# Kernel tuning notes

Hardware: AMD Instinct MI355X
Metric: run time of the kernel (lower is better)

Reference implementation:

```python
import jax, jax.numpy as jnp
import numpy as np

N, E, B = 100000, 200000, 4096
D, FEAT, L = 300, 512, 5
NUM_ATOM, NUM_CHI = 119, 3
NUM_BOND, NUM_DIR = 5, 3
EPS = 1e-5


def setup_inputs() -> dict:
    key = jax.random.key(0)
    ks = jax.random.split(key, 24)
    x = jax.random.randint(ks[0], (N, 2), 0, 3, dtype=jnp.int32)
    edge_index = jax.random.randint(ks[1], (2, E), 0, N, dtype=jnp.int32)
    edge_attr = jax.random.randint(ks[2], (E, 2), 0, 3, dtype=jnp.int32)
    batch = jnp.sort(jax.random.randint(ks[3], (N,), 0, B, dtype=jnp.int32))
    s = 0.02
    p = {
        'x_emb1': jax.random.normal(ks[4], (NUM_ATOM, D)) * s,
        'x_emb2': jax.random.normal(ks[5], (NUM_CHI, D)) * s,
        'edge_emb1': jax.random.normal(ks[6], (L, NUM_BOND, D)) * s,
        'edge_emb2': jax.random.normal(ks[7], (L, NUM_DIR, D)) * s,
        'W1': jax.random.normal(ks[8], (L, D, 2 * D)) * s,
        'b1': jnp.zeros((L, 2 * D)),
        'W2': jax.random.normal(ks[9], (L, 2 * D, D)) * s,
        'b2': jnp.zeros((L, D)),
        'gamma': jnp.ones((L, D)),
        'beta': jnp.zeros((L, D)),
        'W_feat': jax.random.normal(ks[10], (D, FEAT)) * s,
        'b_feat': jnp.zeros((FEAT,)),
        'Wp1': jax.random.normal(ks[11], (FEAT, FEAT // 2)) * s,
        'bp1': jnp.zeros((FEAT // 2,)),
        'Wp2': jax.random.normal(ks[12], (FEAT // 2, FEAT // 2)) * s,
        'bp2': jnp.zeros((FEAT // 2,)),
        'Wp3': jax.random.normal(ks[13], (FEAT // 2, 2)) * s,
        'bp3': jnp.zeros((2,)),
    }
    return dict(x=x, edge_index=edge_index, edge_attr=edge_attr, batch=batch, **p)


def reference(x, edge_index, edge_attr, batch, x_emb1, x_emb2, edge_emb1, edge_emb2,
              W1, b1, W2, b2, gamma, beta, W_feat, b_feat, Wp1, bp1, Wp2, bp2, Wp3, bp3):
    n = x.shape[0]
    ar = jnp.arange(n, dtype=edge_index.dtype)
    src = jnp.concatenate([edge_index[0], ar])  # [E+N] message sources
    dst = jnp.concatenate([edge_index[1], ar])  # [E+N] aggregation targets
    # self-loop edge attr: bond type 4, direction 0
    sl = jnp.stack([jnp.full((n,), 4, edge_attr.dtype), jnp.zeros((n,), edge_attr.dtype)], axis=1)
    ea = jnp.concatenate([edge_attr, sl], axis=0)  # [E+N, 2]

    h = x_emb1[x[:, 0]] + x_emb2[x[:, 1]]  # [N, D]
    for l in range(L):
        ee = edge_emb1[l][ea[:, 0]] + edge_emb2[l][ea[:, 1]]  # [E+N, D]
        msg = h[src] + ee
        aggr = jax.ops.segment_sum(msg, dst, num_segments=n)  # GIN add-aggregate
        h = jax.nn.relu(aggr @ W1[l] + b1[l]) @ W2[l] + b2[l]
        mu = h.mean(axis=0)
        var = ((h - mu) ** 2).mean(axis=0)  # biased var (torch BN training mode)
        h = (h - mu) * jax.lax.rsqrt(var + EPS) * gamma[l] + beta[l]
        if l < L - 1:
            h = jax.nn.relu(h)

    ones = jnp.ones((n,), h.dtype)
    counts = jax.ops.segment_sum(ones, batch, num_segments=B)
    pooled = jax.ops.segment_sum(h, batch, num_segments=B) / jnp.maximum(counts, 1.0)[:, None]
    hf = pooled @ W_feat + b_feat  # [B, FEAT]
    p = jax.nn.softplus(hf @ Wp1 + bp1)
    p = jax.nn.softplus(p @ Wp2 + bp2)
    pred = p @ Wp3 + bp3  # [B, 2]
    return hf, pred
```

## Files before the change

kernel.cpp:

```cpp
#include <hip/hip_runtime.h>
#include <cstdint>
#include <cstddef>

typedef unsigned short u16;
typedef __bf16 bf16x8 __attribute__((ext_vector_type(8)));
typedef float  f32x4  __attribute__((ext_vector_type(4)));

#define NN 100000
#define EE 200000
#define BG 4096
#define DV 300
#define DP 320
#define D2 600
#define D2P 640
#define FEAT 512
#define FH 256
#define NL 5
#define CHUNK 50048
#define QN (NN/4)

__device__ __forceinline__ float b2f(u16 u) {
    union { float f; unsigned int i; } x; x.i = ((unsigned int)u) << 16; return x.f;
}
__device__ __forceinline__ u16 f2b(float f) {
    union { float f; unsigned int i; } x; x.f = f;
    unsigned int r = (x.i + 0x7FFFu + ((x.i >> 16) & 1u)) >> 16;
    return (u16)r;
}
__device__ __forceinline__ float ldp(const void* p, size_t i, int m) {
    return m ? ((const float*)p)[i] : b2f(((const u16*)p)[i]);
}

__global__ void detect_kernel(const void* w1raw, int* mode) {
    if (threadIdx.x != 0 || blockIdx.x != 0) return;
    const u16* p = (const u16*)w1raw;
    int cnt = 0;
    for (int i = 0; i < 128; ++i) {
        u16 v = p[2 * i];
        int e = (v >> 7) & 0xFF;
        if (e >= 100 && e <= 135) ++cnt;
    }
    *mode = (cnt >= 100) ? 0 : 1;
}

__global__ void zero_int_kernel(int* __restrict__ p, long n) {
    long i = (long)blockIdx.x * blockDim.x + threadIdx.x;
    long stride = (long)gridDim.x * blockDim.x;
    for (; i < n; i += stride) p[i] = 0;
}

__global__ void zero_stats_kernel(float* __restrict__ a, float* __restrict__ b) {
    int t = threadIdx.x; a[t] = 0.f; b[t] = 0.f;
}

__global__ void pack_kernel(const void* __restrict__ W1, const void* __restrict__ W2,
                            const void* __restrict__ Wf, const void* __restrict__ Wp1,
                            const void* __restrict__ Wp2,
                            const void* __restrict__ b1, const void* __restrict__ b2,
                            const void* __restrict__ bfe, const void* __restrict__ bp1,
                            const void* __restrict__ bp2,
                            const void* __restrict__ eemb1, const void* __restrict__ eemb2,
                            u16* __restrict__ W1pT, u16* __restrict__ W2pT,
                            u16* __restrict__ WfT, u16* __restrict__ Wp1T, u16* __restrict__ Wp2T,
                            float* __restrict__ b1p, float* __restrict__ b2p,
                            float* __restrict__ bfp, float* __restrict__ bp1p, float* __restrict__ bp2p,
                            const int* __restrict__ modep)
{
    const int m = *modep;
    const int s1 = NL*D2P*DP, s2 = NL*DP*D2P, s3 = FEAT*DP, s4 = FH*FEAT, s5 = FH*FH;
    const int s6 = NL*D2P, s7 = NL*DP, s8 = FEAT, s9 = FH, s10 = FH;
    int idx = blockIdx.x * 256 + threadIdx.x;
    if (idx < s1) {
        int l = idx / (D2P*DP), r = idx % (D2P*DP), n = r / DP, k = r % DP;
        u16 v = 0;
        if (n < D2) {
            if (k < DV) v = f2b(ldp(W1, ((size_t)l*DV + k)*D2 + n, m));
            else if (k < DV + 8) {
                int b = k - DV;
                float acc = 0.f;
                for (int d = 0; d < DV; ++d) {
                    float e = (b < 5) ? ldp(eemb1, ((size_t)l*5 + b)*DV + d, m)
                                      : ldp(eemb2, ((size_t)l*3 + (b-5))*DV + d, m);
                    acc += e * ldp(W1, ((size_t)l*DV + d)*D2 + n, m);
                }
                v = f2b(acc);
            }
        }
        W1pT[idx] = v; return;
    } idx -= s1;
    if (idx < s2) {
        int l = idx / (DP*D2P), r = idx % (DP*D2P), n = r / D2P, k = r % D2P;
        W2pT[idx] = (n < DV && k < D2) ? f2b(ldp(W2, ((size_t)l*D2 + k)*DV + n, m)) : (u16)0; return;
    } idx -= s2;
    if (idx < s3) { int n = idx / DP, k = idx % DP;
        WfT[idx] = (k < DV) ? f2b(ldp(Wf, (size_t)k*FEAT + n, m)) : (u16)0; return; } idx -= s3;
    if (idx < s4) { int n = idx / FEAT, k = idx % FEAT;
        Wp1T[idx] = f2b(ldp(Wp1, (size_t)k*FH + n, m)); return; } idx -= s4;
    if (idx < s5) { int n = idx / FH, k = idx % FH;
        Wp2T[idx] = f2b(ldp(Wp2, (size_t)k*FH + n, m)); return; } idx -= s5;
    if (idx < s6) { int l = idx / D2P, n = idx % D2P;
        b1p[idx] = (n < D2) ? ldp(b1, l*D2 + n, m) : 0.f; return; } idx -= s6;
    if (idx < s7) { int l = idx / DP, n = idx % DP;
        b2p[idx] = (n < DV) ? ldp(b2, l*DV + n, m) : 0.f; return; } idx -= s7;
    if (idx < s8) { bfp[idx] = ldp(bfe, idx, m); return; } idx -= s8;
    if (idx < s9) { bp1p[idx] = ldp(bp1, idx, m); return; } idx -= s9;
    if (idx < s10) { bp2p[idx] = ldp(bp2, idx, m); return; }
}

__global__ void count_kernel(const int* __restrict__ ei, const int* __restrict__ ea,
                             int* __restrict__ indeg, int* __restrict__ cnt)
{
    int e = blockIdx.x * 256 + threadIdx.x;
    if (e >= EE) return;
    int dst = ei[EE + e];
    atomicAdd(&indeg[dst], 1);
    atomicAdd(&cnt[dst*8 + ea[e*2]], 1);
    atomicAdd(&cnt[dst*8 + 5 + ea[e*2+1]], 1);
}

__global__ void scan1_kernel(const int* __restrict__ in, int* __restrict__ out,
                             int* __restrict__ partials, int n)
{
    __shared__ int sm[256];
    int t = threadIdx.x, gi = blockIdx.x * 256 + t;
    int v = (gi < n) ? in[gi] : 0;
    sm[t] = v; __syncthreads();
    int acc = v;
    for (int off = 1; off < 256; off <<= 1) {
        int other = (t >= off) ? sm[t - off] : 0;
        __syncthreads();
        acc += other; sm[t] = acc;
        __syncthreads();
    }
    if (gi < n) out[gi] = acc - v;
    if (t == 255) partials[blockIdx.x] = acc;
}

__global__ void scan2_kernel(int* __restrict__ partials, int nb)
{
    __shared__ int sm[512];
    int t = threadIdx.x;
    int v = (t < nb) ? partials[t] : 0;
    sm[t] = v; __syncthreads();
    int acc = v;
    for (int off = 1; off < 512; off <<= 1) {
        int other = (t >= off) ? sm[t - off] : 0;
        __syncthreads();
        acc += other; sm[t] = acc;
        __syncthreads();
    }
    if (t < nb) partials[t] = acc - v;
}

__global__ void scan3_kernel(int* __restrict__ rowptr, const int* __restrict__ partials,
                             int* __restrict__ cursor, int n)
{
    int i = blockIdx.x * 256 + threadIdx.x;
    if (i < n) {
        int v = rowptr[i] + partials[i >> 8];
        rowptr[i] = v; cursor[i] = v;
    }
    if (i == n) rowptr[n] = EE;
}

__global__ void fill_kernel(const int* __restrict__ ei, int* __restrict__ cursor,
                            int* __restrict__ colidx)
{
    int e = blockIdx.x * 256 + threadIdx.x;
    if (e >= EE) return;
    int src = ei[e], dst = ei[EE + e];
    int pos = atomicAdd(&cursor[dst], 1);
    colidx[pos] = src;
}

__global__ void h0_kernel(const int* __restrict__ x, const void* __restrict__ e1,
                          const void* __restrict__ e2, u16* __restrict__ H,
                          const int* __restrict__ modep)
{
    const int m = *modep;
    int i = blockIdx.x, d = threadIdx.x;
    u16 r = 0;
    if (d < DV) {
        int a = x[i*2], b = x[i*2+1];
        r = f2b(ldp(e1, (size_t)a*DV + d, m) + ldp(e2, (size_t)b*DV + d, m));
    }
    H[(size_t)i*DP + d] = r;
}

template<bool BN>
__global__ __launch_bounds__(320)
void aggr_kernel(const u16* __restrict__ H, const int* __restrict__ rowptr,
                 const int* __restrict__ colidx, const int* __restrict__ cnt,
                 const float* __restrict__ sc, const float* __restrict__ sh,
                 u16* __restrict__ out)
{
    const int b = blockIdx.x, d = threadIdx.x;
    int node[4];
    #pragma unroll
    for (int k = 0; k < 4; ++k) node[k] = b + k * QN;

    if (d < DV) {
        float scv = BN ? sc[d] : 1.f, shv = BN ? sh[d] : 0.f;
        float acc[4];
        int e0[4], deg[4]; int maxdeg = 0;
        #pragma unroll
        for (int k = 0; k < 4; ++k) {
            e0[k] = rowptr[node[k]];
            deg[k] = rowptr[node[k] + 1] - e0[k];
            maxdeg = max(maxdeg, deg[k]);
            float h = b2f(H[(size_t)node[k]*DP + d]);
            if (BN) h = fmaxf(h * scv + shv, 0.f);
            acc[k] = h;
        }
        for (int j = 0; j < maxdeg; ++j) {
            int idx[4];
            #pragma unroll
            for (int k = 0; k < 4; ++k) {
                int jj = e0[k] + j; if (jj > EE - 1) jj = EE - 1;
                idx[k] = (j < deg[k]) ? colidx[jj] : node[k];
            }
            float hv[4];
            #pragma unroll
            for (int k = 0; k < 4; ++k) hv[k] = b2f(H[(size_t)idx[k]*DP + d]);
            #pragma unroll
            for (int k = 0; k < 4; ++k) {
                float h = hv[k];
                if (BN) h = fmaxf(h * scv + shv, 0.f);
                if (j < deg[k]) acc[k] += h;
            }
        }
        #pragma unroll
        for (int k = 0; k < 4; ++k) out[(size_t)node[k]*DP + d] = f2b(acc[k]);
    } else {
        #pragma unroll
        for (int k = 0; k < 4; ++k) {
            float v = 0.f;
            if (d < DV + 8) {
                int c = cnt[node[k]*8 + (d - DV)];
                if (d == DV + 4 || d == DV + 5) c += 1;
                v = (float)c;
            }
            out[(size_t)node[k]*DP + d] = f2b(v);
        }
    }
}

template<int EPI, bool F32OUT, bool STATS>
__global__ __launch_bounds__(256)
void gemm_bt(const u16* __restrict__ A, int lda,
             const u16* __restrict__ Bt,
             const float* __restrict__ bias,
             u16* __restrict__ C, float* __restrict__ Cf, int ldc,
             int M, int Ncols, int K,
             float* __restrict__ cs, float* __restrict__ cs2)
{
    const int MT = (M + 127) >> 7, NT = (Ncols + 127) >> 7;
    const int total = MT * NT;
    {
        int id = blockIdx.x;
        int nper = (total + 7) >> 3;
        int slot = (id & 7) * nper + (id >> 3);
        if (slot >= total) return;
        __shared__ int dummy; (void)dummy;
        int mt_i = slot / NT, nt_i = slot % NT;
        const int m0 = mt_i * 128;
        const int n0 = nt_i * 128;

    __shared__ __align__(16) u16 As[128*64];
    __shared__ __align__(16) u16 Bs[128*64];
    const int t = threadIdx.x;
    const int w = t >> 6, l = t & 63;
    const int wm = (w & 1) * 64, wn = (w >> 1) * 64;
    const int srow = l >> 3;
    const int sg   = ((l & 7) ^ srow) * 8;
    const int fr = l & 15, q = l >> 4;

    f32x4 acc[4][4] = {};

    for (int k0 = 0; k0 < K; k0 += 64) {
        #pragma unroll
        for (int i = 0; i < 8; ++i) {
            int cc = w * 8 + i;
            int rl = (cc & 15) * 8 + srow;
            if (cc < 16) {
                int row = m0 + rl; if (row >= M) row = M - 1;
                const u16* gp = A + (size_t)row * lda + (k0 + sg);
                u16* lp = As + cc * 512;
                __builtin_amdgcn_global_load_lds((__attribute__((address_space(1))) void*)gp,
                                                 (__attribute__((address_space(3))) void*)lp, 16, 0, 0);
            } else {
                int row = n0 + rl; if (row >= Ncols) row = Ncols - 1;
                const u16* gp = Bt + (size_t)row * K + (k0 + sg);
                u16* lp = Bs + (cc - 16) * 512;
                __builtin_amdgcn_global_load_lds((__attribute__((address_space(1))) void*)gp,
                                                 (__attribute__((address_space(3))) void*)lp, 16, 0, 0);
            }
        }
        asm volatile("s_waitcnt vmcnt(0)" ::: "memory");
        __syncthreads();

        #pragma unroll
        for (int s = 0; s < 2; ++s) {
            bf16x8 af[4], bv[4];
            #pragma unroll
            for (int mi = 0; mi < 4; ++mi) {
                int R = wm + mi*16 + fr;
                int g = (s*4 + q) ^ (R & 7);
                af[mi] = *reinterpret_cast<const bf16x8*>(As + R*64 + g*8);
            }
            #pragma unroll
            for (int ni = 0; ni < 4; ++ni) {
                int R = wn + ni*16 + fr;
                int g = (s*4 + q) ^ (R & 7);
                bv[ni] = *reinterpret_cast<const bf16x8*>(Bs + R*64 + g*8);
            }
            #pragma unroll
            for (int mi = 0; mi < 4; ++mi)
                #pragma unroll
                for (int ni = 0; ni < 4; ++ni)
                    acc[mi][ni] = __builtin_amdgcn_mfma_f32_16x16x32_bf16(af[mi], bv[ni], acc[mi][ni], 0, 0, 0);
        }
        __syncthreads();
    }

    const int orow = (l >> 4) * 4, ocol = l & 15;
    #pragma unroll
    for (int ni = 0; ni < 4; ++ni) {
        int col = n0 + wn + ni*16 + ocol;
        if (col >= Ncols) continue;
        float bvv = bias[col];
        float s = 0.f, s2 = 0.f;
        #pragma unroll
        for (int mi = 0; mi < 4; ++mi) {
            #pragma unroll
            for (int r = 0; r < 4; ++r) {
                int row = m0 + wm + mi*16 + orow + r;
                if (row < M) {
                    float v = acc[mi][ni][r] + bvv;
                    if (EPI == 1) v = fmaxf(v, 0.f);
                    else if (EPI == 2) v = fmaxf(v, 0.f) + log1pf(expf(-fabsf(v)));
                    C[(size_t)row * ldc + col] = f2b(v);
                    if (F32OUT) Cf[(size_t)row * ldc + col] = v;
                    if (STATS) { s += v; s2 += v * v; }
                }
            }
        }
        if (STATS) {
            s  += __shfl_xor(s, 16);  s  += __shfl_xor(s, 32);
            s2 += __shfl_xor(s2, 16); s2 += __shfl_xor(s2, 32);
            if ((l >> 4) == 0) {
                atomicAdd(&cs[col], s);
                atomicAdd(&cs2[col], s2);
            }
        }
    }
    }
}

__global__ void bn_finalize(const float* __restrict__ cs, const float* __restrict__ cs2,
                            const void* __restrict__ gamma, const void* __restrict__ beta,
                            int goff, float* __restrict__ sc, float* __restrict__ sh,
                            const int* __restrict__ modep)
{
    const int m = *modep;
    int d = threadIdx.x;
    float a = 0.f, bb = 0.f;
    if (d < DV) {
        float mu = cs[d] / (float)NN;
        float var = cs2[d] / (float)NN - mu * mu;
        var = fmaxf(var, 0.f);
        a = ldp(gamma, goff + d, m) * rsqrtf(var + 1e-5f);
        bb = ldp(beta, goff + d, m) - mu * a;
    }
    sc[d] = a; sh[d] = bb;
}

__global__ void gstart_kernel(const int* __restrict__ batch, int* __restrict__ gs)
{
    int i = blockIdx.x * 256 + threadIdx.x;
    if (i >= NN) return;
    int b = batch[i];
    int pb = (i == 0) ? -1 : batch[i-1];
    for (int g = pb + 1; g <= b; ++g) gs[g] = i;
    if (i == NN - 1) for (int g = b + 1; g <= BG; ++g) gs[g] = NN;
}

__global__ __launch_bounds__(256)
void pool_kernel(const u16* __restrict__ H, const int* __restrict__ gs,
                 const float* __restrict__ sc, const float* __restrict__ sh,
                 u16* __restrict__ pooled)
{
    __shared__ float red[4][320];
    int b = blockIdx.x;
    int wv = threadIdx.x >> 6, lane = threadIdx.x & 63;
    int s = gs[b], e = gs[b+1];
    if (lane < 40) {
        int d0 = lane * 8;
        float a[8] = {0.f,0.f,0.f,0.f,0.f,0.f,0.f,0.f};
        for (int r = s + wv; r < e; r += 4) {
            uint4 row = *(const uint4*)(H + (size_t)r * DP + d0);
            const u16* p = (const u16*)&row;
            #pragma unroll
            for (int j = 0; j < 8; ++j) a[j] += b2f(p[j]);
        }
        #pragma unroll
        for (int j = 0; j < 8; ++j) red[wv][d0 + j] = a[j];
    }
    __syncthreads();
    if (wv == 0 && lane < 40) {
        int d0 = lane * 8;
        int c = e - s; if (c < 1) c = 1;
        float inv = 1.f / (float)c;
        union { uint4 v; u16 o[8]; } pk;
        #pragma unroll
        for (int j = 0; j < 8; ++j) {
            int d = d0 + j;
            float m = (red[0][d] + red[1][d] + red[2][d] + red[3][d]) * inv;
            pk.o[j] = f2b(m * sc[d] + sh[d]);
        }
        *(uint4*)(pooled + (size_t)b * DP + d0) = pk.v;
    }
}

__global__ void pred_kernel(const u16* __restrict__ P2, const void* __restrict__ W3,
                            const void* __restrict__ b3, float* __restrict__ out,
                            const int* __restrict__ modep)
{
    const int m = *modep;
    int r = blockIdx.x, l = threadIdx.x;
    float a0 = 0.f, a1 = 0.f;
    for (int k = l; k < FH; k += 64) {
        float p = b2f(P2[(size_t)r*FH + k]);
        a0 += p * ldp(W3, k*2, m);
        a1 += p * ldp(W3, k*2 + 1, m);
    }
    for (int o = 32; o > 0; o >>= 1) {
        a0 += __shfl_down(a0, o);
        a1 += __shfl_down(a1, o);
    }
    if (l == 0) {
        out[(size_t)r*2]     = a0 + ldp(b3, 0, m);
        out[(size_t)r*2 + 1] = a1 + ldp(b3, 1, m);
    }
}

static inline int gemm_grid(int M, int Ncols) {
    int total = ((M + 127) / 128) * ((Ncols + 127) / 128);
    return ((total + 7) / 8) * 8;
}

extern "C" void kernel_launch(void* const* d_in, const int* in_sizes, int n_in,
                              void* d_out, int out_size, void* d_ws, size_t ws_size,
                              hipStream_t stream)
{
    const int* x      = (const int*)d_in[0];
    const int* ei     = (const int*)d_in[1];
    const int* ea     = (const int*)d_in[2];
    const int* batch  = (const int*)d_in[3];
    const void* x_emb1 = d_in[4];
    const void* x_emb2 = d_in[5];
    const void* eemb1  = d_in[6];
    const void* eemb2  = d_in[7];
    const void* W1     = d_in[8];
    const void* b1     = d_in[9];
    const void* W2     = d_in[10];
    const void* b2     = d_in[11];
    const void* gamma  = d_in[12];
    const void* beta   = d_in[13];
    const void* Wf     = d_in[14];
    const void* bfe    = d_in[15];
    const void* Wp1    = d_in[16];
    const void* bp1    = d_in[17];
    const void* Wp2    = d_in[18];
    const void* bp2    = d_in[19];
    const void* Wp3    = d_in[20];
    const void* bp3    = d_in[21];
    float* outf = (float*)d_out;

    char* ws = (char*)d_ws;
    size_t off = 0;
    auto carve = [&](size_t bytes) -> char* {
        size_t a = (off + 255) & ~(size_t)255; off = a + bytes; return ws + a;
    };

    u16* H      = (u16*)carve((size_t)NN * DP * 2);
    u16* AGGR   = (u16*)carve((size_t)NN * DP * 2);
    u16* T      = (u16*)carve((size_t)CHUNK * D2P * 2);
    u16* POOLED = (u16*)carve((size_t)BG * DP * 2);
    u16* HFB    = (u16*)carve((size_t)BG * FEAT * 2);
    u16* P1     = (u16*)carve((size_t)BG * FH * 2);
    u16* P2     = (u16*)carve((size_t)BG * FH * 2);
    u16* W1pT   = (u16*)carve((size_t)NL * D2P * DP * 2);
    u16* W2pT   = (u16*)carve((size_t)NL * DP * D2P * 2);
    u16* WfT    = (u16*)carve((size_t)FEAT * DP * 2);
    u16* Wp1T   = (u16*)carve((size_t)FH * FEAT * 2);
    u16* Wp2T   = (u16*)carve((size_t)FH * FH * 2);
    float* B1P  = (float*)carve((size_t)NL * D2P * 4);
    float* B2P  = (float*)carve((size_t)NL * DP * 4);
    float* BFP  = (float*)carve((size_t)FEAT * 4);
    float* BP1P = (float*)carve((size_t)FH * 4);
    float* BP2P = (float*)carve((size_t)FH * 4);
    int* INDEG  = (int*)carve((size_t)9 * NN * 4);
    int* CNT    = INDEG + NN;
    int* ROWPTR = (int*)carve((size_t)(NN + 1) * 4);
    int* CURSOR = (int*)carve((size_t)NN * 4);
    int* COLIDX = (int*)carve((size_t)EE * 4);
    int* PART   = (int*)carve(512 * 4);
    float* CS   = (float*)carve(DP * 4);
    float* CS2  = (float*)carve(DP * 4);
    float* BNSC = (float*)carve((size_t)NL * DP * 4);
    float* BNSH = (float*)carve((size_t)NL * DP * 4);
    int* GS     = (int*)carve((size_t)(BG + 1) * 4);
    int* MODEP  = (int*)carve(4);
    (void)ws_size; (void)in_sizes; (void)n_in; (void)out_size;

    detect_kernel<<<1, 64, 0, stream>>>(W1, MODEP);

    const int PACK_TOTAL = NL*D2P*DP + NL*DP*D2P + FEAT*DP + FH*FEAT + FH*FH
                         + NL*D2P + NL*DP + FEAT + FH + FH;
    pack_kernel<<<(PACK_TOTAL + 255)/256, 256, 0, stream>>>(
        W1, W2, Wf, Wp1, Wp2, b1, b2, bfe, bp1, bp2, eemb1, eemb2,
        W1pT, W2pT, WfT, Wp1T, Wp2T, B1P, B2P, BFP, BP1P, BP2P, MODEP);

    zero_int_kernel<<<2048, 256, 0, stream>>>(INDEG, (long)9 * NN);
    count_kernel<<<(EE + 255)/256, 256, 0, stream>>>(ei, ea, INDEG, CNT);

    const int NB = (NN + 255) / 256;
    scan1_kernel<<<NB, 256, 0, stream>>>(INDEG, ROWPTR, PART, NN);
    scan2_kernel<<<1, 512, 0, stream>>>(PART, NB);
    scan3_kernel<<<(NN + 256)/256, 256, 0, stream>>>(ROWPTR, PART, CURSOR, NN);
    fill_kernel<<<(EE + 255)/256, 256, 0, stream>>>(ei, CURSOR, COLIDX);

    h0_kernel<<<NN, DP, 0, stream>>>(x, x_emb1, x_emb2, H, MODEP);
    gstart_kernel<<<(NN + 255)/256, 256, 0, stream>>>(batch, GS);

    for (int l = 0; l < NL; ++l) {
        if (l == 0)
            aggr_kernel<false><<<QN, DP, 0, stream>>>(H, ROWPTR, COLIDX, CNT,
                                                      nullptr, nullptr, AGGR);
        else
            aggr_kernel<true><<<QN, DP, 0, stream>>>(H, ROWPTR, COLIDX, CNT,
                                                     BNSC + (l-1)*DP, BNSH + (l-1)*DP, AGGR);
        zero_stats_kernel<<<1, DP, 0, stream>>>(CS, CS2);
        for (int r0 = 0; r0 < NN; r0 += CHUNK) {
            int mc = NN - r0; if (mc > CHUNK) mc = CHUNK;
            gemm_bt<1,false,false><<<gemm_grid(mc, D2P), 256, 0, stream>>>(
                AGGR + (size_t)r0*DP, DP, W1pT + (size_t)l*D2P*DP,
                B1P + l*D2P, T, nullptr, D2P, mc, D2P, DP, nullptr, nullptr);
            gemm_bt<0,false,true><<<gemm_grid(mc, DP), 256, 0, stream>>>(
                T, D2P, W2pT + (size_t)l*DP*D2P,
                B2P + l*DP, H + (size_t)r0*DP, nullptr, DP, mc, DP, D2P, CS, CS2);
        }
        bn_finalize<<<1, DP, 0, stream>>>(CS, CS2, gamma, beta, l*DV,
                                          BNSC + l*DP, BNSH + l*DP, MODEP);
    }

    pool_kernel<<<BG, 256, 0, stream>>>(H, GS, BNSC + 4*DP, BNSH + 4*DP, POOLED);
    gemm_bt<0,true,false><<<gemm_grid(BG, FEAT), 256, 0, stream>>>(
        POOLED, DP, WfT, BFP, HFB, outf, FEAT, BG, FEAT, DP, nullptr, nullptr);
    gemm_bt<2,false,false><<<gemm_grid(BG, FH), 256, 0, stream>>>(
        HFB, FEAT, Wp1T, BP1P, P1, nullptr, FH, BG, FH, FEAT, nullptr, nullptr);
    gemm_bt<2,false,false><<<gemm_grid(BG, FH), 256, 0, stream>>>(
        P1, FH, Wp2T, BP2P, P2, nullptr, FH, BG, FH, FH, nullptr, nullptr);
    pred_kernel<<<BG, 64, 0, stream>>>(P2, Wp3, bp3, outf + (size_t)BG*FEAT, MODEP);
}
```

Baseline: 1.850 ms.

## Use 2-wave GEMM blocks with 64x128 warp tiles and split out edge-embedding fold

The GEMM now runs with 128 threads per block. Each wave computes a 64x128 output tile (4x8 MFMA accumulators) instead of 64x64, which doubles register accumulators per wave but halves the LDS B-fragment reads per MFMA. Each thread now issues both A and B loads. Separately, the embedding-into-W1 fold moves from the pack kernel into its own kernel. There, a block caches one embedding row in shared memory, so the slow per-element serial loop inside the huge pack grid is gone. The risk is higher VGPR pressure and lower occupancy, and with only 2 waves per block there is less latency hiding.

Result: slower. 2.847 ms (+53.8%).

```diff
diff --git a/kernel.cpp b/kernel.cpp
--- a/kernel.cpp
+++ b/kernel.cpp
@@ -59,7 +59,6 @@
                             const void* __restrict__ b1, const void* __restrict__ b2,
                             const void* __restrict__ bfe, const void* __restrict__ bp1,
                             const void* __restrict__ bp2,
-                            const void* __restrict__ eemb1, const void* __restrict__ eemb2,
                             u16* __restrict__ W1pT, u16* __restrict__ W2pT,
                             u16* __restrict__ WfT, u16* __restrict__ Wp1T, u16* __restrict__ Wp2T,
                             float* __restrict__ b1p, float* __restrict__ b2p,
@@ -75,16 +74,7 @@
         u16 v = 0;
         if (n < D2) {
             if (k < DV) v = f2b(ldp(W1, ((size_t)l*DV + k)*D2 + n, m));
-            else if (k < DV + 8) {
-                int b = k - DV;
-                float acc = 0.f;
-                for (int d = 0; d < DV; ++d) {
-                    float e = (b < 5) ? ldp(eemb1, ((size_t)l*5 + b)*DV + d, m)
-                                      : ldp(eemb2, ((size_t)l*3 + (b-5))*DV + d, m);
-                    acc += e * ldp(W1, ((size_t)l*DV + d)*D2 + n, m);
-                }
-                v = f2b(acc);
-            }
+            else if (k < DV + 8) return;
         }
         W1pT[idx] = v; return;
     } idx -= s1;
@@ -107,6 +97,26 @@
     if (idx < s10) { bp2p[idx] = ldp(bp2, idx, m); return; }
 }
 
+__global__ void fold_kernel(const void* __restrict__ W1,
+                            const void* __restrict__ eemb1, const void* __restrict__ eemb2,
+                            u16* __restrict__ W1pT, const int* __restrict__ modep)
+{
+    const int m = *modep;
+    __shared__ float e[DV];
+    int b = blockIdx.x;
+    int l = b >> 3, bin = b & 7;
+    int n = threadIdx.x;
+    for (int d = n; d < DV; d += 640)
+        e[d] = (bin < 5) ? ldp(eemb1, ((size_t)l*5 + bin)*DV + d, m)
+                         : ldp(eemb2, ((size_t)l*3 + (bin-5))*DV + d, m);
+    __syncthreads();
+    if (n >= D2) return;
+    float acc = 0.f;
+    for (int d = 0; d < DV; ++d)
+        acc += e[d] * ldp(W1, ((size_t)l*DV + d)*D2 + n, m);
+    W1pT[((size_t)l*D2P + n)*DP + DV + bin] = f2b(acc);
+}
+
 __global__ void count_kernel(const int* __restrict__ ei, const int* __restrict__ ea,
                              int* __restrict__ indeg, int* __restrict__ cnt)
 {
@@ -246,7 +256,7 @@
 }
 
 template<int EPI, bool F32OUT, bool STATS>
-__global__ __launch_bounds__(256)
+__global__ __launch_bounds__(128)
 void gemm_bt(const u16* __restrict__ A, int lda,
              const u16* __restrict__ Bt,
              const float* __restrict__ bias,
@@ -256,44 +266,40 @@
 {
     const int MT = (M + 127) >> 7, NT = (Ncols + 127) >> 7;
     const int total = MT * NT;
-    {
-        int id = blockIdx.x;
-        int nper = (total + 7) >> 3;
-        int slot = (id & 7) * nper + (id >> 3);
-        if (slot >= total) return;
-        __shared__ int dummy; (void)dummy;
-        int mt_i = slot / NT, nt_i = slot % NT;
-        const int m0 = mt_i * 128;
-        const int n0 = nt_i * 128;
+    int id = blockIdx.x;
+    int nper = (total + 7) >> 3;
+    int slot = (id & 7) * nper + (id >> 3);
+    if (slot >= total) return;
+    const int m0 = (slot / NT) * 128;
+    const int n0 = (slot % NT) * 128;
 
     __shared__ __align__(16) u16 As[128*64];
     __shared__ __align__(16) u16 Bs[128*64];
     const int t = threadIdx.x;
     const int w = t >> 6, l = t & 63;
-    const int wm = (w & 1) * 64, wn = (w >> 1) * 64;
+    const int wm = w * 64;
     const int srow = l >> 3;
     const int sg   = ((l & 7) ^ srow) * 8;
     const int fr = l & 15, q = l >> 4;
 
-    f32x4 acc[4][4] = {};
+    f32x4 acc[4][8] = {};
 
     for (int k0 = 0; k0 < K; k0 += 64) {
         #pragma unroll
         for (int i = 0; i < 8; ++i) {
             int cc = w * 8 + i;
-            int rl = (cc & 15) * 8 + srow;
-            if (cc < 16) {
+            int rl = cc * 8 + srow;
+            {
                 int row = m0 + rl; if (row >= M) row = M - 1;
                 const u16* gp = A + (size_t)row * lda + (k0 + sg);
-                u16* lp = As + cc * 512;
                 __builtin_amdgcn_global_load_lds((__attribute__((address_space(1))) void*)gp,
-                                                 (__attribute__((address_space(3))) void*)lp, 16, 0, 0);
-            } else {
+                                                 (__attribute__((address_space(3))) void*)(As + cc*512), 16, 0, 0);
+            }
+            {
                 int row = n0 + rl; if (row >= Ncols) row = Ncols - 1;
                 const u16* gp = Bt + (size_t)row * K + (k0 + sg);
-                u16* lp = Bs + (cc - 16) * 512;
                 __builtin_amdgcn_global_load_lds((__attribute__((address_space(1))) void*)gp,
-                                                 (__attribute__((address_space(3))) void*)lp, 16, 0, 0);
+                                                 (__attribute__((address_space(3))) void*)(Bs + cc*512), 16, 0, 0);
             }
         }
         asm volatile("s_waitcnt vmcnt(0)" ::: "memory");
@@ -301,7 +307,7 @@
 
         #pragma unroll
         for (int s = 0; s < 2; ++s) {
-            bf16x8 af[4], bv[4];
+            bf16x8 af[4], bv[8];
             #pragma unroll
             for (int mi = 0; mi < 4; ++mi) {
                 int R = wm + mi*16 + fr;
@@ -309,24 +315,24 @@
                 af[mi] = *reinterpret_cast<const bf16x8*>(As + R*64 + g*8);
             }
             #pragma unroll
-            for (int ni = 0; ni < 4; ++ni) {
-                int R = wn + ni*16 + fr;
+            for (int ni = 0; ni < 8; ++ni) {
+                int R = ni*16 + fr;
                 int g = (s*4 + q) ^ (R & 7);
                 bv[ni] = *reinterpret_cast<const bf16x8*>(Bs + R*64 + g*8);
             }
             #pragma unroll
             for (int mi = 0; mi < 4; ++mi)
                 #pragma unroll
-                for (int ni = 0; ni < 4; ++ni)
+                for (int ni = 0; ni < 8; ++ni)
                     acc[mi][ni] = __builtin_amdgcn_mfma_f32_16x16x32_bf16(af[mi], bv[ni], acc[mi][ni], 0, 0, 0);
         }
         __syncthreads();
     }
 
-    const int orow = (l >> 4) * 4, ocol = l & 15;
+    const int orow = q * 4, ocol = l & 15;
     #pragma unroll
-    for (int ni = 0; ni < 4; ++ni) {
-        int col = n0 + wn + ni*16 + ocol;
+    for (int ni = 0; ni < 8; ++ni) {
+        int col = n0 + ni*16 + ocol;
         if (col >= Ncols) continue;
         float bvv = bias[col];
         float s = 0.f, s2 = 0.f;
@@ -348,12 +354,11 @@
         if (STATS) {
             s  += __shfl_xor(s, 16);  s  += __shfl_xor(s, 32);
             s2 += __shfl_xor(s2, 16); s2 += __shfl_xor(s2, 32);
-            if ((l >> 4) == 0) {
+            if (q == 0) {
                 atomicAdd(&cs[col], s);
                 atomicAdd(&cs2[col], s2);
             }
         }
-    }
     }
 }
 
@@ -519,8 +524,9 @@
     const int PACK_TOTAL = NL*D2P*DP + NL*DP*D2P + FEAT*DP + FH*FEAT + FH*FH
                          + NL*D2P + NL*DP + FEAT + FH + FH;
     pack_kernel<<<(PACK_TOTAL + 255)/256, 256, 0, stream>>>(
-        W1, W2, Wf, Wp1, Wp2, b1, b2, bfe, bp1, bp2, eemb1, eemb2,
+        W1, W2, Wf, Wp1, Wp2, b1, b2, bfe, bp1, bp2,
         W1pT, W2pT, WfT, Wp1T, Wp2T, B1P, B2P, BFP, BP1P, BP2P, MODEP);
+    fold_kernel<<<NL*8, 640, 0, stream>>>(W1, eemb1, eemb2, W1pT, MODEP);
 
     zero_int_kernel<<<2048, 256, 0, stream>>>(INDEG, (long)9 * NN);
     count_kernel<<<(EE + 255)/256, 256, 0, stream>>>(ei, ea, INDEG, CNT);
@@ -544,10 +550,10 @@
         zero_stats_kernel<<<1, DP, 0, stream>>>(CS, CS2);
         for (int r0 = 0; r0 < NN; r0 += CHUNK) {
             int mc = NN - r0; if (mc > CHUNK) mc = CHUNK;
-            gemm_bt<1,false,false><<<gemm_grid(mc, D2P), 256, 0, stream>>>(
+            gemm_bt<1,false,false><<<gemm_grid(mc, D2P), 128, 0, stream>>>(
                 AGGR + (size_t)r0*DP, DP, W1pT + (size_t)l*D2P*DP,
                 B1P + l*D2P, T, nullptr, D2P, mc, D2P, DP, nullptr, nullptr);
-            gemm_bt<0,false,true><<<gemm_grid(mc, DP), 256, 0, stream>>>(
+            gemm_bt<0,false,true><<<gemm_grid(mc, DP), 128, 0, stream>>>(
                 T, D2P, W2pT + (size_t)l*DP*D2P,
                 B2P + l*DP, H + (size_t)r0*DP, nullptr, DP, mc, DP, D2P, CS, CS2);
         }
@@ -556,11 +562,11 @@
     }
 
     pool_kernel<<<BG, 256, 0, stream>>>(H, GS, BNSC + 4*DP, BNSH + 4*DP, POOLED);
-    gemm_bt<0,true,false><<<gemm_grid(BG, FEAT), 256, 0, stream>>>(
+    gemm_bt<0,true,false><<<gemm_grid(BG, FEAT), 128, 0, stream>>>(
         POOLED, DP, WfT, BFP, HFB, outf, FEAT, BG, FEAT, DP, nullptr, nullptr);
-    gemm_bt<2,false,false><<<gemm_grid(BG, FH), 256, 0, stream>>>(
+    gemm_bt<2,false,false><<<gemm_grid(BG, FH), 128, 0, stream>>>(
         HFB, FEAT, Wp1T, BP1P, P1, nullptr, FH, BG, FH, FEAT, nullptr, nullptr);
-    gemm_bt<2,false,false><<<gemm_grid(BG, FH), 256, 0, stream>>>(
+    gemm_bt<2,false,false><<<gemm_grid(BG, FH), 128, 0, stream>>>(
         P1, FH, Wp2T, BP2P, P2, nullptr, FH, BG, FH, FH, nullptr, nullptr);
     pred_kernel<<<BG, 64, 0, stream>>>(P2, Wp3, bp3, outf + (size_t)BG*FEAT, MODEP);
 }
```
